# Kernel optimization log

Hardware: AMD Instinct MI355X
Metric: run time of the kernel (lower is better)

Reference implementation:

```python
import jax, jax.numpy as jnp
import numpy as np

S, N, MSA_DIM, PAIR_DIM, D, H = 8, 256, 256, 128, 32, 8
EPS = 1e-5


def layer_norm(x, w, b):
    mu = jnp.mean(x, axis=-1, keepdims=True)
    var = jnp.mean((x - mu) ** 2, axis=-1, keepdims=True)
    return (x - mu) * jax.lax.rsqrt(var + EPS) * w + b


def setup_inputs() -> dict:
    key = jax.random.key(0)
    ks = jax.random.split(key, 8)
    def rnd(k, shape, scale=1.0):
        return jax.random.normal(k, shape, jnp.float32) * scale
    return {
        "msa_rep": rnd(ks[0], (S, N, MSA_DIM)),
        "pair_rep": rnd(ks[1], (N, N, PAIR_DIM)),
        "ln_w": jnp.ones((MSA_DIM,), jnp.float32),
        "ln_b": jnp.zeros((MSA_DIM,), jnp.float32),
        "w_qkv": rnd(ks[2], (MSA_DIM, 3 * H * D), 0.02),
        "ln_pair_w": jnp.ones((PAIR_DIM,), jnp.float32),
        "ln_pair_b": jnp.zeros((PAIR_DIM,), jnp.float32),
        "w_b": rnd(ks[3], (PAIR_DIM, H), 0.02),
        "w_g": rnd(ks[4], (MSA_DIM, H * D), 0.02),
        "w_out": rnd(ks[5], (H * D, MSA_DIM), 0.02),
        "b_out": jnp.zeros((MSA_DIM,), jnp.float32),
    }


def reference(msa_rep, pair_rep, ln_w, ln_b, w_qkv, ln_pair_w, ln_pair_b,
              w_b, w_g, w_out, b_out):
    s, n, _ = msa_rep.shape
    x = layer_norm(msa_rep, ln_w, ln_b)                      # [s, n, msa_dim]
    qkv = x @ w_qkv                                          # [s, n, 3*h*d]
    # chunk(3, dim=-1) then view(..., d, h): d outer, h inner
    q, k, v = [t.reshape(s, n, D, H) for t in jnp.split(qkv, 3, axis=-1)]
    # pair bias: LN + linear -> [n, n, h], broadcast to [1, i, j, 1, h]
    b = layer_norm(pair_rep, ln_pair_w, ln_pair_b) @ w_b     # [n, n, h]
    g = jax.nn.sigmoid(x @ w_g).reshape(s, n, D, H)          # gate [s, n, d, h]
    # NOTE: logits keep the d axis (no contraction): einsum 'sidh,sjdh->sijdh'
    scores = (q[:, :, None, :, :] * k[:, None, :, :, :]) * (D ** -0.5) \
             + b[None, :, :, None, :]                        # [s, i, j, d, h]
    a = jax.nn.softmax(scores, axis=2)                       # softmax over j
    out = g * jnp.einsum('sijdh,sjdh->sidh', a, v)           # [s, n, d, h]
    return out.reshape(s, n, D * H) @ w_out + b_out          # [s, n, msa_dim]
```

## Files before the change

kernel.cpp:

```cpp
#include <hip/hip_runtime.h>
#include <math.h>

#define S_DIM 8
#define N_RES 256
#define MSA_DIM 256
#define PAIR_DIM 128
#define D_DIM 32
#define H_DIM 8
#define M_ROWS (S_DIM * N_RES)
#define QKV_N (3 * H_DIM * D_DIM)
#define HD (H_DIM * D_DIM)
#define XW_N 1024
#define LOG2E 1.4426950408889634f

typedef __attribute__((ext_vector_type(8))) short short8;
typedef __attribute__((ext_vector_type(4))) float floatx4;

#define DPP_ADD(x, ctrl, rmask)                                                \
    x += __int_as_float(__builtin_amdgcn_update_dpp(                           \
        0, __float_as_int(x), (ctrl), (rmask), 0xf, true))

__device__ __forceinline__ float wave_sum63(float x) {
    DPP_ADD(x, 0x111, 0xf);
    DPP_ADD(x, 0x112, 0xf);
    DPP_ADD(x, 0x114, 0xf);
    DPP_ADD(x, 0x118, 0xf);
    DPP_ADD(x, 0x142, 0xa);
    DPP_ADD(x, 0x143, 0xc);
    return x;
}

__device__ __forceinline__ float quad_sum(float x) {
    x += __int_as_float(__builtin_amdgcn_update_dpp(
        0, __float_as_int(x), 0xB1, 0xf, 0xf, true));
    x += __int_as_float(__builtin_amdgcn_update_dpp(
        0, __float_as_int(x), 0x4E, 0xf, 0xf, true));
    return x;
}

__device__ __forceinline__ unsigned short bf16rn(float v) {
    unsigned u = __float_as_uint(v);
    return (unsigned short)((u + 0x7FFF + ((u >> 16) & 1)) >> 16);
}

__global__ __launch_bounds__(256) void ln_msa_kernel(
    const float* __restrict__ msa, const float* __restrict__ w,
    const float* __restrict__ b, unsigned short* __restrict__ xhi,
    unsigned short* __restrict__ xlo)
{
    int row = blockIdx.x;
    int t = threadIdx.x;
    float v = msa[row * MSA_DIM + t];
    float s1 = wave_sum63(v);
    float s2 = wave_sum63(v * v);
    __shared__ float r1[4], r2[4];
    int wave = t >> 6, lane = t & 63;
    if (lane == 63) { r1[wave] = s1; r2[wave] = s2; }
    __syncthreads();
    float S1 = r1[0] + r1[1] + r1[2] + r1[3];
    float S2 = r2[0] + r2[1] + r2[2] + r2[3];
    float mu = S1 * (1.0f / 256.0f);
    float var = S2 * (1.0f / 256.0f) - mu * mu;
    float rs = rsqrtf(var + 1e-5f);
    float y = (v - mu) * rs * w[t] + b[t];
    unsigned short h = bf16rn(y);
    float hf = __uint_as_float((unsigned)h << 16);
    unsigned short l = bf16rn(y - hf);
    xhi[row * 256 + t] = h;
    xlo[row * 256 + t] = l;
}

__global__ __launch_bounds__(256) void wconv_kernel(
    const float* __restrict__ w_qkv, const float* __restrict__ w_g,
    unsigned short* __restrict__ whiT, unsigned short* __restrict__ wloT)
{
    int id = blockIdx.x * 256 + threadIdx.x;
    int n = id >> 5, oct = id & 31;
    int k0 = oct * 8;
    const float* src;
    int stride;
    if (n < QKV_N) { src = w_qkv + n; stride = QKV_N; }
    else           { src = w_g + (n - QKV_N); stride = HD; }
    unsigned short h8[8], l8[8];
#pragma unroll
    for (int j = 0; j < 8; j++) {
        float v = src[(size_t)(k0 + j) * stride];
        unsigned short h = bf16rn(v);
        float hf = __uint_as_float((unsigned)h << 16);
        h8[j] = h;
        l8[j] = bf16rn(v - hf);
    }
    *(short8*)&whiT[n * 256 + k0] = *(short8*)h8;
    *(short8*)&wloT[n * 256 + k0] = *(short8*)l8;
}

__global__ __launch_bounds__(256) void xw_mfma_kernel(
    const unsigned short* __restrict__ xhi, const unsigned short* __restrict__ xlo,
    const unsigned short* __restrict__ whiT, const unsigned short* __restrict__ wloT,
    float* __restrict__ q_t, float* __restrict__ k_t,
    float* __restrict__ v_t, float* __restrict__ g_t)
{
    __shared__ unsigned short As[64 * 72];
    __shared__ unsigned short Bs[128 * 72];
    __shared__ float Cs[64 * 132];
    int t = threadIdx.x;
    int n0 = blockIdx.x * 128, m0 = blockIdx.y * 64;
    int w = t >> 6, L = t & 63;
    int wm = (w & 1) * 32, wn = (w >> 1) * 64;
    int l15 = L & 15, l4 = L >> 4;

    int alm = t >> 3, alk = (t & 7) * 8;
    floatx4 acc[2][4];
#pragma unroll
    for (int a = 0; a < 2; a++)
#pragma unroll
        for (int b = 0; b < 4; b++) acc[a][b] = (floatx4){0, 0, 0, 0};

    const unsigned short* Asrc = xhi;
    const unsigned short* Bsrc = whiT;
    short8 pa0 = *(const short8*)&Asrc[(m0 + alm) * 256 + alk];
    short8 pa1 = *(const short8*)&Asrc[(m0 + alm + 32) * 256 + alk];
    short8 pb[4];
#pragma unroll
    for (int j = 0; j < 4; j++) {
        int id = t + 256 * j;
        int bn = id >> 3, bc = (id & 7) * 8;
        pb[j] = *(const short8*)&Bsrc[(n0 + bn) * 256 + bc];
    }

    for (int r = 0; r < 12; r++) {
        __syncthreads();
        *(short8*)&As[alm * 72 + alk] = pa0;
        *(short8*)&As[(alm + 32) * 72 + alk] = pa1;
#pragma unroll
        for (int j = 0; j < 4; j++) {
            int id = t + 256 * j;
            int bn = id >> 3, bc = (id & 7) * 8;
            *(short8*)&Bs[bn * 72 + bc] = pb[j];
        }
        __syncthreads();
        if (r < 11) {
            int rn = r + 1;
            int seg = rn >> 2, kb = (rn & 3) * 64;
            const unsigned short* An = (seg == 1) ? xlo : xhi;
            const unsigned short* Bn = (seg == 2) ? wloT : whiT;
            pa0 = *(const short8*)&An[(m0 + alm) * 256 + kb + alk];
            pa1 = *(const short8*)&An[(m0 + alm + 32) * 256 + kb + alk];
#pragma unroll
            for (int j = 0; j < 4; j++) {
                int id = t + 256 * j;
                int bn = id >> 3, bc = (id & 7) * 8;
                pb[j] = *(const short8*)&Bn[(n0 + bn) * 256 + kb + bc];
            }
        }
#pragma unroll
        for (int ks = 0; ks < 2; ks++) {
            int ko = ks * 32 + l4 * 8;
            short8 af[2], bf[4];
#pragma unroll
            for (int a = 0; a < 2; a++)
                af[a] = *(short8*)&As[(wm + a * 16 + l15) * 72 + ko];
#pragma unroll
            for (int b = 0; b < 4; b++)
                bf[b] = *(short8*)&Bs[(wn + b * 16 + l15) * 72 + ko];
#pragma unroll
            for (int a = 0; a < 2; a++)
#pragma unroll
                for (int b = 0; b < 4; b++)
                    acc[a][b] = __builtin_amdgcn_mfma_f32_16x16x32_bf16(
                        af[a], bf[b], acc[a][b], 0, 0, 0);
        }
    }

#pragma unroll
    for (int a = 0; a < 2; a++)
#pragma unroll
        for (int b = 0; b < 4; b++) {
            int nl = wn + b * 16 + l15;
#pragma unroll
            for (int rg = 0; rg < 4; rg++) {
                int ml = wm + a * 16 + l4 * 4 + rg;
                Cs[ml * 132 + nl] = acc[a][b][rg];
            }
        }
    __syncthreads();
    int qkv_mode = (n0 < QKV_N);
    int chunk = n0 >> 8;
    int dbase = (n0 & 255) >> 3;
#pragma unroll
    for (int j = 0; j < 8; j++) {
        int id = t + 256 * j;
        int m = id >> 5;
        int h = (id >> 2) & 7;
        int dq = id & 3;
        float vals[4];
#pragma unroll
        for (int jj = 0; jj < 4; jj++)
            vals[jj] = Cs[m * 132 + (dq * 4 + jj) * 8 + h];
        int mm = m0 + m;
        int daddr = dbase + dq * 4;
        if (qkv_mode) {
            float* dst = (chunk == 0) ? q_t : ((chunk == 1) ? k_t : v_t);
            *(float4*)&dst[(size_t)(h * M_ROWS + mm) * D_DIM + daddr] =
                *(float4*)vals;
        } else {
            float4 o;
            o.x = 1.0f / (1.0f + __expf(-vals[0]));
            o.y = 1.0f / (1.0f + __expf(-vals[1]));
            o.z = 1.0f / (1.0f + __expf(-vals[2]));
            o.w = 1.0f / (1.0f + __expf(-vals[3]));
            *(float4*)&g_t[(size_t)(h * M_ROWS + mm) * D_DIM + daddr] = o;
        }
    }
}

__global__ __launch_bounds__(256) void out_gemm_kernel(
    const float* __restrict__ X, const float* __restrict__ W,
    float* __restrict__ part)
{
    __shared__ float Xs[16][68];
    __shared__ float Ws[16][132];
    int t = threadIdx.x;
    int n0 = blockIdx.x * 128;
    int m0 = blockIdx.y * 64;
    int k0g = blockIdx.z * 64;
    int tm = t >> 4, tn = t & 15;
    int lxm = t >> 2, lxk = (t & 3) * 4;
    int lwk = t >> 4, lwn = (t & 15) * 8;
    float acc[4][8] = {};
    int wr0 = ((k0g + lwk) & 31) * 8 + ((k0g + lwk) >> 5);
    float4 xa = *(const float4*)&X[(m0 + lxm) * 256 + k0g + lxk];
    float4 w0 = *(const float4*)&W[(size_t)wr0 * 256 + n0 + lwn];
    float4 w1 = *(const float4*)&W[(size_t)wr0 * 256 + n0 + lwn + 4];
    for (int kt = 0; kt < 4; kt++) {
        __syncthreads();
        Xs[lxk + 0][lxm] = xa.x; Xs[lxk + 1][lxm] = xa.y;
        Xs[lxk + 2][lxm] = xa.z; Xs[lxk + 3][lxm] = xa.w;
        *(float4*)&Ws[lwk][lwn] = w0;
        *(float4*)&Ws[lwk][lwn + 4] = w1;
        __syncthreads();
        if (kt < 3) {
            int kb = k0g + (kt + 1) * 16;
            int wrow = ((kb + lwk) & 31) * 8 + ((kb + lwk) >> 5);
            xa = *(const float4*)&X[(m0 + lxm) * 256 + kb + lxk];
            w0 = *(const float4*)&W[(size_t)wrow * 256 + n0 + lwn];
            w1 = *(const float4*)&W[(size_t)wrow * 256 + n0 + lwn + 4];
        }
#pragma unroll
        for (int kk = 0; kk < 16; kk++) {
            float a[4], b[8];
            *(float4*)a = *(const float4*)&Xs[kk][tm * 4];
            *(float4*)&b[0] = *(const float4*)&Ws[kk][tn * 4];
            *(float4*)&b[4] = *(const float4*)&Ws[kk][64 + tn * 4];
#pragma unroll
            for (int i = 0; i < 4; i++)
#pragma unroll
                for (int u = 0; u < 8; u++) acc[i][u] += a[i] * b[u];
        }
    }
    float* pb = part + (size_t)blockIdx.z * (M_ROWS * 256);
#pragma unroll
    for (int i = 0; i < 4; i++) {
        int mm = m0 + tm * 4 + i;
        *(float4*)&pb[mm * 256 + n0 + tn * 4] = *(float4*)&acc[i][0];
        *(float4*)&pb[mm * 256 + n0 + 64 + tn * 4] = *(float4*)&acc[i][4];
    }
}

__global__ __launch_bounds__(256) void reduce_out_kernel(
    const float* __restrict__ part, const float* __restrict__ bias,
    float* __restrict__ out)
{
    int idx = blockIdx.x * 256 + threadIdx.x;
    int e = idx * 4;
    int n = e & 255;
    float4 p0 = *(const float4*)&part[e];
    float4 p1 = *(const float4*)&part[e + M_ROWS * 256];
    float4 p2 = *(const float4*)&part[e + 2 * M_ROWS * 256];
    float4 p3 = *(const float4*)&part[e + 3 * M_ROWS * 256];
    float4 bb = *(const float4*)&bias[n];
    float4 o;
    o.x = p0.x + p1.x + p2.x + p3.x + bb.x;
    o.y = p0.y + p1.y + p2.y + p3.y + bb.y;
    o.z = p0.z + p1.z + p2.z + p3.z + bb.z;
    o.w = p0.w + p1.w + p2.w + p3.w + bb.w;
    *(float4*)&out[e] = o;
}

__global__ __launch_bounds__(128) void pb_setup_kernel(
    const float* __restrict__ lw, const float* __restrict__ lb,
    const float* __restrict__ wb, float* __restrict__ Abuf)
{
    __shared__ float P[128][8], Q[128][8];
    int c = threadIdx.x;
    float lwc = lw[c], lbc = lb[c];
#pragma unroll
    for (int h = 0; h < 8; h++) {
        float w = wb[c * 8 + h];
        float a = lwc * w;
        P[c][h] = a;
        Q[c][h] = lbc * w;
        Abuf[c * 12 + h] = a * LOG2E;
    }
    __syncthreads();
    if (c < 8) {
        float s = 0, cc = 0;
        for (int k = 0; k < 128; k++) { s += P[k][c]; cc += Q[k][c]; }
        Abuf[1536 + c] = s * LOG2E;
        Abuf[1544 + c] = cc * LOG2E;
    }
}

__global__ __launch_bounds__(256) void pair_bias_kernel(
    const float* __restrict__ pair, const float* __restrict__ Abuf,
    float* __restrict__ b2)
{
    __shared__ __align__(16) float As[1552];
    int t = threadIdx.x;
    for (int idx = t; idx < 388; idx += 256)
        ((float4*)As)[idx] = ((const float4*)Abuf)[idx];
    __syncthreads();
    int row = blockIdx.x * 64 + (t >> 2);
    int q = t & 3;
    const float* in = pair + (size_t)row * PAIR_DIM;
    float4 x4[8];
#pragma unroll
    for (int it = 0; it < 8; it++)
        x4[it] = *(const float4*)&in[it * 16 + q * 4];
    float s = 0, s2 = 0;
    float dot[8] = {};
#pragma unroll
    for (int it = 0; it < 8; it++) {
        float xk[4];
        *(float4*)xk = x4[it];
#pragma unroll
        for (int k = 0; k < 4; k++) {
            int c = it * 16 + q * 4 + k;
            float xv = xk[k];
            s += xv; s2 += xv * xv;
            float4 A0 = *(const float4*)&As[c * 12];
            float4 A1 = *(const float4*)&As[c * 12 + 4];
            dot[0] += xv * A0.x; dot[1] += xv * A0.y;
            dot[2] += xv * A0.z; dot[3] += xv * A0.w;
            dot[4] += xv * A1.x; dot[5] += xv * A1.y;
            dot[6] += xv * A1.z; dot[7] += xv * A1.w;
        }
    }
    s = quad_sum(s);
    s2 = quad_sum(s2);
#pragma unroll
    for (int h = 0; h < 8; h++) dot[h] = quad_sum(dot[h]);
    float mu = s * (1.0f / 128.0f);
    float var = s2 * (1.0f / 128.0f) - mu * mu;
    float rs = rsqrtf(var + 1e-5f);
    int h0 = q * 2;
#pragma unroll
    for (int u = 0; u < 2; u++) {
        int h = h0 + u;
        b2[h * 65536 + row] = rs * (dot[h] - mu * As[1536 + h]) + As[1544 + h];
    }
}

__global__ __launch_bounds__(256) void attn_kernel(
    const float* __restrict__ q_t, const float* __restrict__ k_t,
    const float* __restrict__ v_t, const float* __restrict__ g_t,
    const float* __restrict__ b2, float* __restrict__ ao)
{
    __shared__ float k_sh[256][32];
    __shared__ float v_sh[256][32];
    int blk = blockIdx.x;
    int s = blk >> 6, h = (blk >> 3) & 7, it = blk & 7;
    int t = threadIdx.x;
    const float* kb = k_t + (size_t)(h * M_ROWS + s * N_RES) * D_DIM;
    const float* vb = v_t + (size_t)(h * M_ROWS + s * N_RES) * D_DIM;
    for (int idx = t; idx < 2048; idx += 256) {
        ((float4*)k_sh)[idx] = ((const float4*)kb)[idx];
        ((float4*)v_sh)[idx] = ((const float4*)vb)[idx];
    }
    __syncthreads();
    int jp = t & 3, dg = (t >> 2) & 7, li = t >> 5;
    int d0 = dg * 4;
    const float SCL2 = 0.17677669529663687f * LOG2E;
    int ig[4], mrow[4];
    float qs[4][4];
#pragma unroll
    for (int r = 0; r < 4; r++) {
        ig[r] = it * 32 + r * 8 + li;
        mrow[r] = s * N_RES + ig[r];
        float4 q4 = *(const float4*)&q_t[(size_t)(h * M_ROWS + mrow[r]) * D_DIM + d0];
        qs[r][0] = q4.x * SCL2; qs[r][1] = q4.y * SCL2;
        qs[r][2] = q4.z * SCL2; qs[r][3] = q4.w * SCL2;
    }
    float den[4][4] = {}, acc[4][4] = {};
    const float* bbase = b2 + h * 65536;
    for (int js4 = 0; js4 < 16; js4++) {
        float bb[4][4];
#pragma unroll
        for (int r = 0; r < 4; r++)
            *(float4*)&bb[r][0] =
                *(const float4*)&bbase[ig[r] * 256 + jp * 64 + js4 * 4];
#pragma unroll
        for (int u = 0; u < 4; u++) {
            int j = jp * 64 + js4 * 4 + u;
            float ka[4], va[4];
            *(float4*)ka = *(const float4*)&k_sh[j][d0];
            *(float4*)va = *(const float4*)&v_sh[j][d0];
#pragma unroll
            for (int r = 0; r < 4; r++) {
#pragma unroll
                for (int c = 0; c < 4; c++) {
                    float e = __builtin_amdgcn_exp2f(qs[r][c] * ka[c] + bb[r][u]);
                    den[r][c] += e;
                    acc[r][c] += e * va[c];
                }
            }
        }
    }
#pragma unroll
    for (int r = 0; r < 4; r++)
#pragma unroll
        for (int c = 0; c < 4; c++) {
            den[r][c] = quad_sum(den[r][c]);
            acc[r][c] = quad_sum(acc[r][c]);
        }
    if (jp == 0) {
#pragma unroll
        for (int r = 0; r < 4; r++) {
            float4 g4 = *(const float4*)&g_t[(size_t)(h * M_ROWS + mrow[r]) * D_DIM + d0];
            float4 o;
            o.x = g4.x * acc[r][0] / den[r][0];
            o.y = g4.y * acc[r][1] / den[r][1];
            o.z = g4.z * acc[r][2] / den[r][2];
            o.w = g4.w * acc[r][3] / den[r][3];
            *(float4*)&ao[(size_t)mrow[r] * HD + h * 32 + d0] = o;
        }
    }
}

extern "C" void kernel_launch(void* const* d_in, const int* in_sizes, int n_in,
                              void* d_out, int out_size, void* d_ws, size_t ws_size,
                              hipStream_t stream)
{
    const float* msa_rep   = (const float*)d_in[0];
    const float* pair_rep  = (const float*)d_in[1];
    const float* ln_w      = (const float*)d_in[2];
    const float* ln_b      = (const float*)d_in[3];
    const float* w_qkv     = (const float*)d_in[4];
    const float* ln_pair_w = (const float*)d_in[5];
    const float* ln_pair_b = (const float*)d_in[6];
    const float* w_b       = (const float*)d_in[7];
    const float* w_g       = (const float*)d_in[8];
    const float* w_out     = (const float*)d_in[9];
    const float* b_out     = (const float*)d_in[10];
    float* out = (float*)d_out;

    float* ws = (float*)d_ws;
    const size_t CH = 524288;
    float* q_t  = ws + 0 * CH;
    float* k_t  = ws + 1 * CH;
    float* v_t  = ws + 2 * CH;
    float* g_t  = ws + 3 * CH;
    float* b2   = ws + 4 * CH;
    float* ao   = ws + 5 * CH;
    float* Abuf = ws + 6 * CH;
    float* part = ws + 7 * CH;
    unsigned short* xhi  = (unsigned short*)(ws + 11 * CH);
    unsigned short* xlo  = xhi + M_ROWS * 256;
    unsigned short* whiT = (unsigned short*)(ws + 12 * CH);
    unsigned short* wloT = whiT + XW_N * 256;

    wconv_kernel<<<128, 256, 0, stream>>>(w_qkv, w_g, whiT, wloT);

    ln_msa_kernel<<<M_ROWS, 256, 0, stream>>>(msa_rep, ln_w, ln_b, xhi, xlo);

    xw_mfma_kernel<<<dim3(8, 32), 256, 0, stream>>>(
        xhi, xlo, whiT, wloT, q_t, k_t, v_t, g_t);

    pb_setup_kernel<<<1, 128, 0, stream>>>(ln_pair_w, ln_pair_b, w_b, Abuf);

    pair_bias_kernel<<<65536 / 64, 256, 0, stream>>>(pair_rep, Abuf, b2);

    attn_kernel<<<512, 256, 0, stream>>>(q_t, k_t, v_t, g_t, b2, ao);

    out_gemm_kernel<<<dim3(2, 32, 4), 256, 0, stream>>>(ao, w_out, part);

    reduce_out_kernel<<<512, 256, 0, stream>>>(part, b_out, out);
}
```

Baseline: 154.7 us.

## Merge prep kernels into one launch and move output GEMM to split-bf16 MFMA

```diff
diff --git a/kernel.cpp b/kernel.cpp
--- a/kernel.cpp
+++ b/kernel.cpp
@@ -43,55 +43,148 @@
     return (unsigned short)((u + 0x7FFF + ((u >> 16) & 1)) >> 16);
 }
 
-__global__ __launch_bounds__(256) void ln_msa_kernel(
-    const float* __restrict__ msa, const float* __restrict__ w,
-    const float* __restrict__ b, unsigned short* __restrict__ xhi,
+__global__ __launch_bounds__(256) void prep_kernel(
+    const float* __restrict__ pair, const float* __restrict__ lw,
+    const float* __restrict__ lb, const float* __restrict__ wb,
+    float* __restrict__ b2,
+    const float* __restrict__ w_qkv, const float* __restrict__ w_g,
+    unsigned short* __restrict__ whiT, unsigned short* __restrict__ wloT,
+    const float* __restrict__ w_out,
+    unsigned short* __restrict__ wouthiT, unsigned short* __restrict__ woutloT,
+    const float* __restrict__ msa, const float* __restrict__ lnw,
+    const float* __restrict__ lnb, unsigned short* __restrict__ xhi,
     unsigned short* __restrict__ xlo)
 {
-    int row = blockIdx.x;
+    __shared__ __align__(16) float shm[2080];
+    int bx = blockIdx.x;
     int t = threadIdx.x;
-    float v = msa[row * MSA_DIM + t];
-    float s1 = wave_sum63(v);
-    float s2 = wave_sum63(v * v);
-    __shared__ float r1[4], r2[4];
-    int wave = t >> 6, lane = t & 63;
-    if (lane == 63) { r1[wave] = s1; r2[wave] = s2; }
-    __syncthreads();
-    float S1 = r1[0] + r1[1] + r1[2] + r1[3];
-    float S2 = r2[0] + r2[1] + r2[2] + r2[3];
-    float mu = S1 * (1.0f / 256.0f);
-    float var = S2 * (1.0f / 256.0f) - mu * mu;
-    float rs = rsqrtf(var + 1e-5f);
-    float y = (v - mu) * rs * w[t] + b[t];
-    unsigned short h = bf16rn(y);
-    float hf = __uint_as_float((unsigned)h << 16);
-    unsigned short l = bf16rn(y - hf);
-    xhi[row * 256 + t] = h;
-    xlo[row * 256 + t] = l;
-}
-
-__global__ __launch_bounds__(256) void wconv_kernel(
-    const float* __restrict__ w_qkv, const float* __restrict__ w_g,
-    unsigned short* __restrict__ whiT, unsigned short* __restrict__ wloT)
-{
-    int id = blockIdx.x * 256 + threadIdx.x;
-    int n = id >> 5, oct = id & 31;
-    int k0 = oct * 8;
-    const float* src;
-    int stride;
-    if (n < QKV_N) { src = w_qkv + n; stride = QKV_N; }
-    else           { src = w_g + (n - QKV_N); stride = HD; }
-    unsigned short h8[8], l8[8];
-#pragma unroll
-    for (int j = 0; j < 8; j++) {
-        float v = src[(size_t)(k0 + j) * stride];
-        unsigned short h = bf16rn(v);
-        float hf = __uint_as_float((unsigned)h << 16);
-        h8[j] = h;
-        l8[j] = bf16rn(v - hf);
-    }
-    *(short8*)&whiT[n * 256 + k0] = *(short8*)h8;
-    *(short8*)&wloT[n * 256 + k0] = *(short8*)l8;
+
+    if (bx < 1024) {
+        float* As = shm;
+        float* Spart = shm + 1552;
+        float* Qpart = shm + 1816;
+        if (t < 128) {
+            float lwc = lw[t];
+#pragma unroll
+            for (int h = 0; h < 8; h++)
+                As[t * 12 + h] = lwc * wb[t * 8 + h] * LOG2E;
+        }
+        __syncthreads();
+        {
+            int h = t >> 5, seg = t & 31, cbase = seg * 4;
+            float sa = 0, sq = 0;
+#pragma unroll
+            for (int cc = 0; cc < 4; cc++) {
+                int c = cbase + cc;
+                sa += As[c * 12 + h];
+                sq += lb[c] * wb[c * 8 + h];
+            }
+            Spart[h * 33 + seg] = sa;
+            Qpart[h * 33 + seg] = sq * LOG2E;
+        }
+        __syncthreads();
+        if (t < 8) {
+            float s = 0, q = 0;
+#pragma unroll
+            for (int j = 0; j < 32; j++) {
+                s += Spart[t * 33 + j];
+                q += Qpart[t * 33 + j];
+            }
+            As[1536 + t] = s;
+            As[1544 + t] = q;
+        }
+        __syncthreads();
+        int row = bx * 64 + (t >> 2);
+        int q = t & 3;
+        const float* in = pair + (size_t)row * PAIR_DIM;
+        float4 x4[8];
+#pragma unroll
+        for (int it = 0; it < 8; it++)
+            x4[it] = *(const float4*)&in[it * 16 + q * 4];
+        float s = 0, s2 = 0;
+        float dot[8] = {};
+#pragma unroll
+        for (int it = 0; it < 8; it++) {
+            float xk[4];
+            *(float4*)xk = x4[it];
+#pragma unroll
+            for (int k = 0; k < 4; k++) {
+                int c = it * 16 + q * 4 + k;
+                float xv = xk[k];
+                s += xv; s2 += xv * xv;
+                float4 A0 = *(const float4*)&As[c * 12];
+                float4 A1 = *(const float4*)&As[c * 12 + 4];
+                dot[0] += xv * A0.x; dot[1] += xv * A0.y;
+                dot[2] += xv * A0.z; dot[3] += xv * A0.w;
+                dot[4] += xv * A1.x; dot[5] += xv * A1.y;
+                dot[6] += xv * A1.z; dot[7] += xv * A1.w;
+            }
+        }
+        s = quad_sum(s);
+        s2 = quad_sum(s2);
+#pragma unroll
+        for (int h = 0; h < 8; h++) dot[h] = quad_sum(dot[h]);
+        float mu = s * (1.0f / 128.0f);
+        float var = s2 * (1.0f / 128.0f) - mu * mu;
+        float rs = rsqrtf(var + 1e-5f);
+        int h0 = q * 2;
+#pragma unroll
+        for (int u = 0; u < 2; u++) {
+            int h = h0 + u;
+            b2[h * 65536 + row] = rs * (dot[h] - mu * As[1536 + h]) + As[1544 + h];
+        }
+    } else if (bx < 1152) {
+        int id = (bx - 1024) * 256 + t;
+        int n = id >> 5, oct = id & 31, k0 = oct * 8;
+        const float* src;
+        int stride;
+        if (n < QKV_N) { src = w_qkv + n; stride = QKV_N; }
+        else           { src = w_g + (n - QKV_N); stride = HD; }
+        unsigned short h8[8], l8[8];
+#pragma unroll
+        for (int j = 0; j < 8; j++) {
+            float v = src[(size_t)(k0 + j) * stride];
+            unsigned short h = bf16rn(v);
+            h8[j] = h;
+            l8[j] = bf16rn(v - __uint_as_float((unsigned)h << 16));
+        }
+        *(short8*)&whiT[n * 256 + k0] = *(short8*)h8;
+        *(short8*)&wloT[n * 256 + k0] = *(short8*)l8;
+    } else if (bx < 1184) {
+        int id = (bx - 1152) * 256 + t;
+        int n = id >> 5, oct = id & 31, k0 = oct * 8;
+        unsigned short h8[8], l8[8];
+#pragma unroll
+        for (int j = 0; j < 8; j++) {
+            int k = k0 + j;
+            int wrow = (k & 31) * 8 + (k >> 5);
+            float v = w_out[(size_t)wrow * 256 + n];
+            unsigned short h = bf16rn(v);
+            h8[j] = h;
+            l8[j] = bf16rn(v - __uint_as_float((unsigned)h << 16));
+        }
+        *(short8*)&wouthiT[n * 256 + k0] = *(short8*)h8;
+        *(short8*)&woutloT[n * 256 + k0] = *(short8*)l8;
+    } else {
+        int row = bx - 1184;
+        float v = msa[row * MSA_DIM + t];
+        float s1 = wave_sum63(v);
+        float s2 = wave_sum63(v * v);
+        float* r1 = shm;
+        float* r2 = shm + 4;
+        int wave = t >> 6, lane = t & 63;
+        if (lane == 63) { r1[wave] = s1; r2[wave] = s2; }
+        __syncthreads();
+        float S1 = r1[0] + r1[1] + r1[2] + r1[3];
+        float S2 = r2[0] + r2[1] + r2[2] + r2[3];
+        float mu = S1 * (1.0f / 256.0f);
+        float var = S2 * (1.0f / 256.0f) - mu * mu;
+        float rs = rsqrtf(var + 1e-5f);
+        float y = (v - mu) * rs * lnw[t] + lnb[t];
+        unsigned short h = bf16rn(y);
+        xhi[row * 256 + t] = h;
+        xlo[row * 256 + t] = bf16rn(y - __uint_as_float((unsigned)h << 16));
+    }
 }
 
 __global__ __launch_bounds__(256) void xw_mfma_kernel(
@@ -108,7 +201,6 @@
     int w = t >> 6, L = t & 63;
     int wm = (w & 1) * 32, wn = (w >> 1) * 64;
     int l15 = L & 15, l4 = L >> 4;
-
     int alm = t >> 3, alk = (t & 7) * 8;
     floatx4 acc[2][4];
 #pragma unroll
@@ -116,16 +208,14 @@
 #pragma unroll
         for (int b = 0; b < 4; b++) acc[a][b] = (floatx4){0, 0, 0, 0};
 
-    const unsigned short* Asrc = xhi;
-    const unsigned short* Bsrc = whiT;
-    short8 pa0 = *(const short8*)&Asrc[(m0 + alm) * 256 + alk];
-    short8 pa1 = *(const short8*)&Asrc[(m0 + alm + 32) * 256 + alk];
+    short8 pa0 = *(const short8*)&xhi[(m0 + alm) * 256 + alk];
+    short8 pa1 = *(const short8*)&xhi[(m0 + alm + 32) * 256 + alk];
     short8 pb[4];
 #pragma unroll
     for (int j = 0; j < 4; j++) {
         int id = t + 256 * j;
         int bn = id >> 3, bc = (id & 7) * 8;
-        pb[j] = *(const short8*)&Bsrc[(n0 + bn) * 256 + bc];
+        pb[j] = *(const short8*)&whiT[(n0 + bn) * 256 + bc];
     }
 
     for (int r = 0; r < 12; r++) {
@@ -171,7 +261,6 @@
                         af[a], bf[b], acc[a][b], 0, 0, 0);
         }
     }
-
 #pragma unroll
     for (int a = 0; a < 2; a++)
 #pragma unroll
@@ -214,157 +303,11 @@
     }
 }
 
-__global__ __launch_bounds__(256) void out_gemm_kernel(
-    const float* __restrict__ X, const float* __restrict__ W,
-    float* __restrict__ part)
-{
-    __shared__ float Xs[16][68];
-    __shared__ float Ws[16][132];
-    int t = threadIdx.x;
-    int n0 = blockIdx.x * 128;
-    int m0 = blockIdx.y * 64;
-    int k0g = blockIdx.z * 64;
-    int tm = t >> 4, tn = t & 15;
-    int lxm = t >> 2, lxk = (t & 3) * 4;
-    int lwk = t >> 4, lwn = (t & 15) * 8;
-    float acc[4][8] = {};
-    int wr0 = ((k0g + lwk) & 31) * 8 + ((k0g + lwk) >> 5);
-    float4 xa = *(const float4*)&X[(m0 + lxm) * 256 + k0g + lxk];
-    float4 w0 = *(const float4*)&W[(size_t)wr0 * 256 + n0 + lwn];
-    float4 w1 = *(const float4*)&W[(size_t)wr0 * 256 + n0 + lwn + 4];
-    for (int kt = 0; kt < 4; kt++) {
-        __syncthreads();
-        Xs[lxk + 0][lxm] = xa.x; Xs[lxk + 1][lxm] = xa.y;
-        Xs[lxk + 2][lxm] = xa.z; Xs[lxk + 3][lxm] = xa.w;
-        *(float4*)&Ws[lwk][lwn] = w0;
-        *(float4*)&Ws[lwk][lwn + 4] = w1;
-        __syncthreads();
-        if (kt < 3) {
-            int kb = k0g + (kt + 1) * 16;
-            int wrow = ((kb + lwk) & 31) * 8 + ((kb + lwk) >> 5);
-            xa = *(const float4*)&X[(m0 + lxm) * 256 + kb + lxk];
-            w0 = *(const float4*)&W[(size_t)wrow * 256 + n0 + lwn];
-            w1 = *(const float4*)&W[(size_t)wrow * 256 + n0 + lwn + 4];
-        }
-#pragma unroll
-        for (int kk = 0; kk < 16; kk++) {
-            float a[4], b[8];
-            *(float4*)a = *(const float4*)&Xs[kk][tm * 4];
-            *(float4*)&b[0] = *(const float4*)&Ws[kk][tn * 4];
-            *(float4*)&b[4] = *(const float4*)&Ws[kk][64 + tn * 4];
-#pragma unroll
-            for (int i = 0; i < 4; i++)
-#pragma unroll
-                for (int u = 0; u < 8; u++) acc[i][u] += a[i] * b[u];
-        }
-    }
-    float* pb = part + (size_t)blockIdx.z * (M_ROWS * 256);
-#pragma unroll
-    for (int i = 0; i < 4; i++) {
-        int mm = m0 + tm * 4 + i;
-        *(float4*)&pb[mm * 256 + n0 + tn * 4] = *(float4*)&acc[i][0];
-        *(float4*)&pb[mm * 256 + n0 + 64 + tn * 4] = *(float4*)&acc[i][4];
-    }
-}
-
-__global__ __launch_bounds__(256) void reduce_out_kernel(
-    const float* __restrict__ part, const float* __restrict__ bias,
-    float* __restrict__ out)
-{
-    int idx = blockIdx.x * 256 + threadIdx.x;
-    int e = idx * 4;
-    int n = e & 255;
-    float4 p0 = *(const float4*)&part[e];
-    float4 p1 = *(const float4*)&part[e + M_ROWS * 256];
-    float4 p2 = *(const float4*)&part[e + 2 * M_ROWS * 256];
-    float4 p3 = *(const float4*)&part[e + 3 * M_ROWS * 256];
-    float4 bb = *(const float4*)&bias[n];
-    float4 o;
-    o.x = p0.x + p1.x + p2.x + p3.x + bb.x;
-    o.y = p0.y + p1.y + p2.y + p3.y + bb.y;
-    o.z = p0.z + p1.z + p2.z + p3.z + bb.z;
-    o.w = p0.w + p1.w + p2.w + p3.w + bb.w;
-    *(float4*)&out[e] = o;
-}
-
-__global__ __launch_bounds__(128) void pb_setup_kernel(
-    const float* __restrict__ lw, const float* __restrict__ lb,
-    const float* __restrict__ wb, float* __restrict__ Abuf)
-{
-    __shared__ float P[128][8], Q[128][8];
-    int c = threadIdx.x;
-    float lwc = lw[c], lbc = lb[c];
-#pragma unroll
-    for (int h = 0; h < 8; h++) {
-        float w = wb[c * 8 + h];
-        float a = lwc * w;
-        P[c][h] = a;
-        Q[c][h] = lbc * w;
-        Abuf[c * 12 + h] = a * LOG2E;
-    }
-    __syncthreads();
-    if (c < 8) {
-        float s = 0, cc = 0;
-        for (int k = 0; k < 128; k++) { s += P[k][c]; cc += Q[k][c]; }
-        Abuf[1536 + c] = s * LOG2E;
-        Abuf[1544 + c] = cc * LOG2E;
-    }
-}
-
-__global__ __launch_bounds__(256) void pair_bias_kernel(
-    const float* __restrict__ pair, const float* __restrict__ Abuf,
-    float* __restrict__ b2)
-{
-    __shared__ __align__(16) float As[1552];
-    int t = threadIdx.x;
-    for (int idx = t; idx < 388; idx += 256)
-        ((float4*)As)[idx] = ((const float4*)Abuf)[idx];
-    __syncthreads();
-    int row = blockIdx.x * 64 + (t >> 2);
-    int q = t & 3;
-    const float* in = pair + (size_t)row * PAIR_DIM;
-    float4 x4[8];
-#pragma unroll
-    for (int it = 0; it < 8; it++)
-        x4[it] = *(const float4*)&in[it * 16 + q * 4];
-    float s = 0, s2 = 0;
-    float dot[8] = {};
-#pragma unroll
-    for (int it = 0; it < 8; it++) {
-        float xk[4];
-        *(float4*)xk = x4[it];
-#pragma unroll
-        for (int k = 0; k < 4; k++) {
-            int c = it * 16 + q * 4 + k;
-            float xv = xk[k];
-            s += xv; s2 += xv * xv;
-            float4 A0 = *(const float4*)&As[c * 12];
-            float4 A1 = *(const float4*)&As[c * 12 + 4];
-            dot[0] += xv * A0.x; dot[1] += xv * A0.y;
-            dot[2] += xv * A0.z; dot[3] += xv * A0.w;
-            dot[4] += xv * A1.x; dot[5] += xv * A1.y;
-            dot[6] += xv * A1.z; dot[7] += xv * A1.w;
-        }
-    }
-    s = quad_sum(s);
-    s2 = quad_sum(s2);
-#pragma unroll
-    for (int h = 0; h < 8; h++) dot[h] = quad_sum(dot[h]);
-    float mu = s * (1.0f / 128.0f);
-    float var = s2 * (1.0f / 128.0f) - mu * mu;
-    float rs = rsqrtf(var + 1e-5f);
-    int h0 = q * 2;
-#pragma unroll
-    for (int u = 0; u < 2; u++) {
-        int h = h0 + u;
-        b2[h * 65536 + row] = rs * (dot[h] - mu * As[1536 + h]) + As[1544 + h];
-    }
-}
-
 __global__ __launch_bounds__(256) void attn_kernel(
     const float* __restrict__ q_t, const float* __restrict__ k_t,
     const float* __restrict__ v_t, const float* __restrict__ g_t,
-    const float* __restrict__ b2, float* __restrict__ ao)
+    const float* __restrict__ b2, unsigned short* __restrict__ ao_hi,
+    unsigned short* __restrict__ ao_lo)
 {
     __shared__ float k_sh[256][32];
     __shared__ float v_sh[256][32];
@@ -427,13 +370,124 @@
 #pragma unroll
         for (int r = 0; r < 4; r++) {
             float4 g4 = *(const float4*)&g_t[(size_t)(h * M_ROWS + mrow[r]) * D_DIM + d0];
-            float4 o;
-            o.x = g4.x * acc[r][0] / den[r][0];
-            o.y = g4.y * acc[r][1] / den[r][1];
-            o.z = g4.z * acc[r][2] / den[r][2];
-            o.w = g4.w * acc[r][3] / den[r][3];
-            *(float4*)&ao[(size_t)mrow[r] * HD + h * 32 + d0] = o;
-        }
+            float o[4];
+            o[0] = g4.x * acc[r][0] / den[r][0];
+            o[1] = g4.y * acc[r][1] / den[r][1];
+            o[2] = g4.z * acc[r][2] / den[r][2];
+            o[3] = g4.w * acc[r][3] / den[r][3];
+            unsigned short hi[4], lo[4];
+#pragma unroll
+            for (int c = 0; c < 4; c++) {
+                hi[c] = bf16rn(o[c]);
+                lo[c] = bf16rn(o[c] - __uint_as_float((unsigned)hi[c] << 16));
+            }
+            size_t base = (size_t)mrow[r] * 256 + h * 32 + d0;
+            uint2 ph, pl;
+            ph.x = (unsigned)hi[0] | ((unsigned)hi[1] << 16);
+            ph.y = (unsigned)hi[2] | ((unsigned)hi[3] << 16);
+            pl.x = (unsigned)lo[0] | ((unsigned)lo[1] << 16);
+            pl.y = (unsigned)lo[2] | ((unsigned)lo[3] << 16);
+            *(uint2*)&ao_hi[base] = ph;
+            *(uint2*)&ao_lo[base] = pl;
+        }
+    }
+}
+
+__global__ __launch_bounds__(256) void out_mfma_kernel(
+    const unsigned short* __restrict__ ahi, const unsigned short* __restrict__ alo,
+    const unsigned short* __restrict__ whi, const unsigned short* __restrict__ wlo,
+    const float* __restrict__ bias, float* __restrict__ out)
+{
+    __shared__ unsigned short As[64 * 72];
+    __shared__ unsigned short Bs[128 * 72];
+    __shared__ float Cs[64 * 132];
+    int t = threadIdx.x;
+    int n0 = blockIdx.x * 128, m0 = blockIdx.y * 64;
+    int w = t >> 6, L = t & 63;
+    int wm = (w & 1) * 32, wn = (w >> 1) * 64;
+    int l15 = L & 15, l4 = L >> 4;
+    int alm = t >> 3, alk = (t & 7) * 8;
+    floatx4 acc[2][4];
+#pragma unroll
+    for (int a = 0; a < 2; a++)
+#pragma unroll
+        for (int b = 0; b < 4; b++) acc[a][b] = (floatx4){0, 0, 0, 0};
+
+    short8 pa0 = *(const short8*)&ahi[(m0 + alm) * 256 + alk];
+    short8 pa1 = *(const short8*)&ahi[(m0 + alm + 32) * 256 + alk];
+    short8 pb[4];
+#pragma unroll
+    for (int j = 0; j < 4; j++) {
+        int id = t + 256 * j;
+        int bn = id >> 3, bc = (id & 7) * 8;
+        pb[j] = *(const short8*)&whi[(n0 + bn) * 256 + bc];
+    }
+
+    for (int r = 0; r < 12; r++) {
+        __syncthreads();
+        *(short8*)&As[alm * 72 + alk] = pa0;
+        *(short8*)&As[(alm + 32) * 72 + alk] = pa1;
+#pragma unroll
+        for (int j = 0; j < 4; j++) {
+            int id = t + 256 * j;
+            int bn = id >> 3, bc = (id & 7) * 8;
+            *(short8*)&Bs[bn * 72 + bc] = pb[j];
+        }
+        __syncthreads();
+        if (r < 11) {
+            int rn = r + 1;
+            int seg = rn >> 2, kb = (rn & 3) * 64;
+            const unsigned short* An = (seg == 1) ? alo : ahi;
+            const unsigned short* Bn = (seg == 2) ? wlo : whi;
+            pa0 = *(const short8*)&An[(m0 + alm) * 256 + kb + alk];
+            pa1 = *(const short8*)&An[(m0 + alm + 32) * 256 + kb + alk];
+#pragma unroll
+            for (int j = 0; j < 4; j++) {
+                int id = t + 256 * j;
+                int bn = id >> 3, bc = (id & 7) * 8;
+                pb[j] = *(const short8*)&Bn[(n0 + bn) * 256 + kb + bc];
+            }
+        }
+#pragma unroll
+        for (int ks = 0; ks < 2; ks++) {
+            int ko = ks * 32 + l4 * 8;
+            short8 af[2], bf[4];
+#pragma unroll
+            for (int a = 0; a < 2; a++)
+                af[a] = *(short8*)&As[(wm + a * 16 + l15) * 72 + ko];
+#pragma unroll
+            for (int b = 0; b < 4; b++)
+                bf[b] = *(short8*)&Bs[(wn + b * 16 + l15) * 72 + ko];
+#pragma unroll
+            for (int a = 0; a < 2; a++)
+#pragma unroll
+                for (int b = 0; b < 4; b++)
+                    acc[a][b] = __builtin_amdgcn_mfma_f32_16x16x32_bf16(
+                        af[a], bf[b], acc[a][b], 0, 0, 0);
+        }
+    }
+#pragma unroll
+    for (int a = 0; a < 2; a++)
+#pragma unroll
+        for (int b = 0; b < 4; b++) {
+            int nl = wn + b * 16 + l15;
+#pragma unroll
+            for (int rg = 0; rg < 4; rg++) {
+                int ml = wm + a * 16 + l4 * 4 + rg;
+                Cs[ml * 132 + nl] = acc[a][b][rg];
+            }
+        }
+    __syncthreads();
+#pragma unroll
+    for (int j = 0; j < 8; j++) {
+        int id = t + 256 * j;
+        int m = id >> 5, nc = (id & 31) * 4;
+        float4 v = *(float4*)&Cs[m * 132 + nc];
+        float4 bb = *(const float4*)&bias[n0 + nc];
+        float4 o;
+        o.x = v.x + bb.x; o.y = v.y + bb.y;
+        o.z = v.z + bb.z; o.w = v.w + bb.w;
+        *(float4*)&out[(size_t)(m0 + m) * 256 + n0 + nc] = o;
     }
 }
 
@@ -456,33 +510,31 @@
 
     float* ws = (float*)d_ws;
     const size_t CH = 524288;
-    float* q_t  = ws + 0 * CH;
-    float* k_t  = ws + 1 * CH;
-    float* v_t  = ws + 2 * CH;
-    float* g_t  = ws + 3 * CH;
-    float* b2   = ws + 4 * CH;
-    float* ao   = ws + 5 * CH;
-    float* Abuf = ws + 6 * CH;
-    float* part = ws + 7 * CH;
-    unsigned short* xhi  = (unsigned short*)(ws + 11 * CH);
-    unsigned short* xlo  = xhi + M_ROWS * 256;
-    unsigned short* whiT = (unsigned short*)(ws + 12 * CH);
-    unsigned short* wloT = whiT + XW_N * 256;
-
-    wconv_kernel<<<128, 256, 0, stream>>>(w_qkv, w_g, whiT, wloT);
-
-    ln_msa_kernel<<<M_ROWS, 256, 0, stream>>>(msa_rep, ln_w, ln_b, xhi, xlo);
+    float* q_t = ws + 0 * CH;
+    float* k_t = ws + 1 * CH;
+    float* v_t = ws + 2 * CH;
+    float* g_t = ws + 3 * CH;
+    float* b2  = ws + 4 * CH;
+    unsigned short* ao_hi   = (unsigned short*)(ws + 5 * CH);
+    unsigned short* ao_lo   = ao_hi + (size_t)M_ROWS * 256;
+    unsigned short* xhi     = (unsigned short*)(ws + 6 * CH);
+    unsigned short* xlo     = xhi + (size_t)M_ROWS * 256;
+    unsigned short* whiT    = (unsigned short*)(ws + 7 * CH);
+    unsigned short* wloT    = whiT + (size_t)XW_N * 256;
+    unsigned short* wouthiT = (unsigned short*)(ws + 8 * CH);
+    unsigned short* woutloT = wouthiT + 65536;
+
+    prep_kernel<<<3232, 256, 0, stream>>>(
+        pair_rep, ln_pair_w, ln_pair_b, w_b, b2,
+        w_qkv, w_g, whiT, wloT,
+        w_out, wouthiT, woutloT,
+        msa_rep, ln_w, ln_b, xhi, xlo);
 
     xw_mfma_kernel<<<dim3(8, 32), 256, 0, stream>>>(
         xhi, xlo, whiT, wloT, q_t, k_t, v_t, g_t);
 
-    pb_setup_kernel<<<1, 128, 0, stream>>>(ln_pair_w, ln_pair_b, w_b, Abuf);
-
-    pair_bias_kernel<<<65536 / 64, 256, 0, stream>>>(pair_rep, Abuf, b2);
-
-    attn_kernel<<<512, 256, 0, stream>>>(q_t, k_t, v_t, g_t, b2, ao);
-
-    out_gemm_kernel<<<dim3(2, 32, 4), 256, 0, stream>>>(ao, w_out, part);
-
-    reduce_out_kernel<<<512, 256, 0, stream>>>(part, b_out, out);
-}
+    attn_kernel<<<512, 256, 0, stream>>>(q_t, k_t, v_t, g_t, b2, ao_hi, ao_lo);
+
+    out_mfma_kernel<<<dim3(2, 32), 256, 0, stream>>>(
+        ao_hi, ao_lo, wouthiT, woutloT, b_out, out);
+}
```

After: 147.6 us. 4.6% less time.
